# Performance work log

Measured on AMD Instinct MI355X. Metric: run time of the kernel, lower is better.

## Reference

```python
import jax, jax.numpy as jnp
import numpy as np

C, H, V, N, T = 1024, 256, 10000, 16, 256


def setup_inputs() -> dict:
    key = jax.random.key(0)
    ks = jax.random.split(key, 16)
    s = 1.0 / np.sqrt(H)
    rn = lambda k, shape, sc: (jax.random.normal(k, shape, dtype=jnp.float32) * sc)
    d = {}
    d["text"] = jax.random.randint(ks[0], (N, T), 0, V)
    d["start_emb"] = rn(ks[1], (C, H), 1.0)
    d["sw1"] = rn(ks[2], (H, H), s); d["sb1"] = jnp.zeros((H,), jnp.float32)
    d["sw2"] = rn(ks[3], (H, H), s); d["sb2"] = jnp.zeros((H,), jnp.float32)
    d["sw3"] = rn(ks[4], (H, 1), s); d["sb3"] = jnp.zeros((1,), jnp.float32)
    d["state_emb"] = rn(ks[5], (C, H), 1.0)
    d["tw1"] = rn(ks[6], (H, H), s); d["tb1"] = jnp.zeros((H,), jnp.float32)
    d["tw2"] = rn(ks[7], (H, H), s); d["tb2"] = jnp.zeros((H,), jnp.float32)
    d["tw3"] = rn(ks[8], (H, C), s); d["tb3"] = jnp.zeros((C,), jnp.float32)
    d["pre_emb"] = rn(ks[9], (C, H), 1.0)
    d["ew1"] = rn(ks[10], (H, H), s); d["eb1"] = jnp.zeros((H,), jnp.float32)
    d["ew2"] = rn(ks[11], (H, H), s); d["eb2"] = jnp.zeros((H,), jnp.float32)
    d["ew3"] = rn(ks[12], (H, V), s); d["eb3"] = jnp.zeros((V,), jnp.float32)
    return d


def _res(x, w1, b1, w2, b2):
    # ResidualLayerOld: relu(lin2(relu(lin1(x)))) + x
    return jax.nn.relu(jax.nn.relu(x @ w1 + b1) @ w2 + b2) + x


def reference(text, start_emb, sw1, sb1, sw2, sb2, sw3, sb3,
              state_emb, tw1, tb1, tw2, tb2, tw3, tb3,
              pre_emb, ew1, eb1, ew2, eb2, ew3, eb3):
    # start: [C] log p(z_0)
    start = jax.nn.log_softmax((_res(start_emb, sw1, sb1, sw2, sb2) @ sw3 + sb3)[:, 0])
    # transition: log_softmax over next state, then permute -> [next, prev]
    trans = jax.nn.log_softmax(_res(state_emb, tw1, tb1, tw2, tb2) @ tw3 + tb3, axis=-1).T
    # emission: log_softmax over vocab, permute -> [V, C]
    emit = jax.nn.log_softmax(_res(pre_emb, ew1, eb1, ew2, eb2) @ ew3 + eb3, axis=-1).T

    obs = emit[text]                      # [N, T, C] log p(x_t | z_t=c)
    alpha0 = start[None, :] + obs[:, 0]   # [N, C]

    def step(alpha, e_t):
        # log-semiring matvec: alpha'[n,j] = logsumexp_i alpha[n,i] + trans[j,i]
        a = jax.scipy.special.logsumexp(alpha[:, None, :] + trans[None, :, :], axis=-1) + e_t
        return a, None

    alpha, _ = jax.lax.scan(step, alpha0, jnp.swapaxes(obs, 0, 1)[1:])
    # evidence: logsumexp over final states, summed over batch (full lengths)
    return jax.scipy.special.logsumexp(alpha, axis=-1).sum()
```

## Files before the change

### kernel.cpp

```cpp
#include <hip/hip_runtime.h>
#include <hip/hip_bf16.h>
#include <cstddef>

#define CC 1024
#define HH 256
#define VV 10000
#define NN 16
#define TT 256
#define NB 16
#define NVB 40

typedef __attribute__((ext_vector_type(8))) short s8b;
typedef __attribute__((ext_vector_type(4))) float f32x4;
typedef __attribute__((ext_vector_type(4))) unsigned int u32x4;

__device__ __forceinline__ unsigned short f2bf(float f) {
    unsigned int b = __builtin_bit_cast(unsigned int, f);
    b += 0x7FFFu + ((b >> 16) & 1u);
    return (unsigned short)(b >> 16);
}
__device__ __forceinline__ float bf2f(unsigned short u) {
    return __builtin_bit_cast(float, ((unsigned int)u) << 16);
}

__global__ __launch_bounds__(256) void k_prep(
    const float* __restrict__ start_emb,
    const float* __restrict__ sw1, const float* __restrict__ sb1,
    const float* __restrict__ sw2, const float* __restrict__ sb2,
    const float* __restrict__ sw3, const float* __restrict__ sb3,
    const float* __restrict__ state_emb,
    const float* __restrict__ tw1, const float* __restrict__ tb1,
    const float* __restrict__ tw2, const float* __restrict__ tb2,
    const float* __restrict__ tw3, const float* __restrict__ tb3,
    const float* __restrict__ pre_emb,
    const float* __restrict__ ew1, const float* __restrict__ eb1,
    const float* __restrict__ ew2, const float* __restrict__ eb2,
    float* __restrict__ res_e, float* __restrict__ slog,
    unsigned short* __restrict__ PB, unsigned short* __restrict__ vbuf)
{
    __shared__ float xs[256][24];
    __shared__ float hs[256][24];
    const int th = threadIdx.x;
    const int b = blockIdx.x;

    if (b < 64) {
        const int r0 = b * 16;
        #pragma unroll
        for (int k = 0; k < 16; k++) xs[th][k] = pre_emb[(size_t)(r0 + k) * HH + th];
        __syncthreads();
        float acc[16];
        float b1v = eb1[th];
        #pragma unroll
        for (int r = 0; r < 16; r++) acc[r] = b1v;
        for (int h = 0; h < HH; h++) {
            float w = ew1[(size_t)h * HH + th];
            #pragma unroll
            for (int r = 0; r < 16; r++) acc[r] = fmaf(xs[h][r], w, acc[r]);
        }
        #pragma unroll
        for (int r = 0; r < 16; r++) hs[th][r] = fmaxf(acc[r], 0.f);
        __syncthreads();
        float b2v = eb2[th];
        #pragma unroll
        for (int r = 0; r < 16; r++) acc[r] = b2v;
        for (int h = 0; h < HH; h++) {
            float w = ew2[(size_t)h * HH + th];
            #pragma unroll
            for (int r = 0; r < 16; r++) acc[r] = fmaf(hs[h][r], w, acc[r]);
        }
        #pragma unroll
        for (int r = 0; r < 16; r++) {
            size_t idx = (size_t)(r0 + r) * HH + th;
            res_e[idx] = fmaxf(acc[r], 0.f) + pre_emb[idx];
        }
    } else if (b < 128) {
        const int r0 = (b - 64) * 16;
        #pragma unroll
        for (int k = 0; k < 16; k++) xs[th][k] = start_emb[(size_t)(r0 + k) * HH + th];
        __syncthreads();
        float acc[16];
        float b1v = sb1[th];
        #pragma unroll
        for (int r = 0; r < 16; r++) acc[r] = b1v;
        for (int h = 0; h < HH; h++) {
            float w = sw1[(size_t)h * HH + th];
            #pragma unroll
            for (int r = 0; r < 16; r++) acc[r] = fmaf(xs[h][r], w, acc[r]);
        }
        #pragma unroll
        for (int r = 0; r < 16; r++) hs[th][r] = fmaxf(acc[r], 0.f);
        __syncthreads();
        float b2v = sb2[th];
        #pragma unroll
        for (int r = 0; r < 16; r++) acc[r] = b2v;
        for (int h = 0; h < HH; h++) {
            float w = sw2[(size_t)h * HH + th];
            #pragma unroll
            for (int r = 0; r < 16; r++) acc[r] = fmaf(hs[h][r], w, acc[r]);
        }
        float accf[16];
        #pragma unroll
        for (int r = 0; r < 16; r++)
            accf[r] = fmaxf(acc[r], 0.f) + start_emb[(size_t)(r0 + r) * HH + th];
        __syncthreads();
        float* ws = (float*)&hs[0][0];
        float wv = sw3[th];
        const int wq = th >> 6, ln = th & 63;
        #pragma unroll
        for (int r = 0; r < 16; r++) {
            float p = accf[r] * wv;
            #pragma unroll
            for (int o = 32; o; o >>= 1) p += __shfl_xor(p, o);
            if (ln == 0) ws[wq * 16 + r] = p;
        }
        __syncthreads();
        if (th < 16) slog[r0 + th] = ws[th] + ws[16 + th] + ws[32 + th] + ws[48 + th] + sb3[0];
    } else if (b < 384) {
        const int r0c = (b - 128) * 4;
        float (*rs)[256] = (float (*)[256])&xs[0][0];
        float (*h2)[256] = (float (*)[256])(&xs[0][0] + 1024);
        float* sred = (float*)&hs[0][0];
        for (int k = 0; k < 4; k++) rs[k][th] = state_emb[(size_t)(r0c + k) * HH + th];
        __syncthreads();
        float a1[4];
        {
            float b1v = tb1[th];
            #pragma unroll
            for (int r = 0; r < 4; r++) a1[r] = b1v;
            for (int h = 0; h < HH; h++) {
                float w = tw1[(size_t)h * HH + th];
                #pragma unroll
                for (int r = 0; r < 4; r++) a1[r] = fmaf(rs[r][h], w, a1[r]);
            }
        }
        #pragma unroll
        for (int r = 0; r < 4; r++) h2[r][th] = fmaxf(a1[r], 0.f);
        __syncthreads();
        float a2[4];
        {
            float b2v = tb2[th];
            #pragma unroll
            for (int r = 0; r < 4; r++) a2[r] = b2v;
            for (int h = 0; h < HH; h++) {
                float w = tw2[(size_t)h * HH + th];
                #pragma unroll
                for (int r = 0; r < 4; r++) a2[r] = fmaf(h2[r][h], w, a2[r]);
            }
        }
        #pragma unroll
        for (int r = 0; r < 4; r++) rs[r][th] = fmaxf(a2[r], 0.f) + rs[r][th];
        __syncthreads();
        float acc[4][4];
        #pragma unroll
        for (int r = 0; r < 4; r++)
            #pragma unroll
            for (int q = 0; q < 4; q++) acc[r][q] = tb3[th + q * 256];
        for (int h = 0; h < HH; h++) {
            float w0 = tw3[(size_t)h * CC + th];
            float w1 = tw3[(size_t)h * CC + th + 256];
            float w2 = tw3[(size_t)h * CC + th + 512];
            float w3 = tw3[(size_t)h * CC + th + 768];
            #pragma unroll
            for (int r = 0; r < 4; r++) {
                float xv = rs[r][h];
                acc[r][0] = fmaf(xv, w0, acc[r][0]);
                acc[r][1] = fmaf(xv, w1, acc[r][1]);
                acc[r][2] = fmaf(xv, w2, acc[r][2]);
                acc[r][3] = fmaf(xv, w3, acc[r][3]);
            }
        }
        for (int r = 0; r < 4; r++) {
            float m = fmaxf(fmaxf(acc[r][0], acc[r][1]), fmaxf(acc[r][2], acc[r][3]));
            sred[th] = m; __syncthreads();
            for (int off = 128; off > 0; off >>= 1) { if (th < off) sred[th] = fmaxf(sred[th], sred[th + off]); __syncthreads(); }
            float rm = sred[0]; __syncthreads();
            float ssum = __expf(acc[r][0] - rm) + __expf(acc[r][1] - rm) + __expf(acc[r][2] - rm) + __expf(acc[r][3] - rm);
            sred[th] = ssum; __syncthreads();
            for (int off = 128; off > 0; off >>= 1) { if (th < off) sred[th] += sred[th + off]; __syncthreads(); }
            float inv = 1.0f / sred[0]; __syncthreads();
            #pragma unroll
            for (int q = 0; q < 4; q++) {
                float p = __expf(acc[r][q] - rm) * inv;
                PB[(size_t)(th + q * 256) * CC + (r0c + r)] = f2bf(p);
            }
        }
    } else {
        const int blk = b - 384;
        unsigned long long* dst = (unsigned long long*)vbuf + (size_t)blk * 16384;
        for (int i = th; i < 16384; i += 256) dst[i] = 0xFFFFFFFFFFFFFFFFull;
    }
}

__global__ __launch_bounds__(256) void k_emitg(const float* __restrict__ res_e,
                                               const float* __restrict__ ew3,
                                               const float* __restrict__ eb3,
                                               unsigned short* __restrict__ emitT,
                                               float* __restrict__ epart2)
{
    const int vb = blockIdx.x, c0 = blockIdx.y * 64;
    const int th = threadIdx.x;
    const int w = th >> 6, l = th & 63;
    const int lhi = l >> 4, llo = l & 15;
    const int wv = w & 1, wc = w >> 1;

    __shared__ __align__(16) unsigned short ewT[64 * 256];
    __shared__ __align__(16) unsigned short rsb[64 * 256];
    __shared__ float ebl[64];
    __shared__ float wlse[4][2][16][2];

    {
        char* base = (char*)rsb;
        #pragma unroll
        for (int i = 0; i < 8; i++) {
            int g = i * 2048 + th * 8;
            int row = g >> 8, h0 = g & 255;
            const float* src = res_e + (size_t)(c0 + row) * HH + h0;
            float4 f0 = *(const float4*)(src);
            float4 f1 = *(const float4*)(src + 4);
            s8b pk;
            pk[0] = (short)f2bf(f0.x); pk[1] = (short)f2bf(f0.y);
            pk[2] = (short)f2bf(f0.z); pk[3] = (short)f2bf(f0.w);
            pk[4] = (short)f2bf(f1.x); pk[5] = (short)f2bf(f1.y);
            pk[6] = (short)f2bf(f1.z); pk[7] = (short)f2bf(f1.w);
            *(s8b*)(base + row * 512 + ((h0 * 2) ^ ((row & 7) << 4))) = pk;
        }
    }

    float rM = -1e30f, rS = 0.f;

    for (int r = 0; r < 4; r++) {
        const int v0r = vb * 256 + r * 64;
        __syncthreads();
        {
            int tv = th & 63;
            char* base = (char*)ewT;
            int rowoff = tv * 512;
            int key = (tv & 7) << 4;
            int vglob = v0r + tv;
            bool valid = vglob < VV;
            #pragma unroll 8
            for (int i = 0; i < 64; i++) {
                int h = (th >> 6) + i * 4;
                float x = valid ? ew3[(size_t)h * VV + vglob] : 0.f;
                *(unsigned short*)(base + rowoff + ((h * 2) ^ key)) = f2bf(x);
            }
        }
        if (th < 64) ebl[th] = (v0r + th < VV) ? eb3[v0r + th] : 0.f;
        __syncthreads();

        f32x4 acc[2][2] = {{{0,0,0,0},{0,0,0,0}},{{0,0,0,0},{0,0,0,0}}};
        const char* ea = (const char*)ewT;
        const char* rb = (const char*)rsb;
        const int arow0 = wv * 32 + llo, arow1 = wv * 32 + 16 + llo;
        const int brow0 = wc * 32 + llo, brow1 = wc * 32 + 16 + llo;
        const int akey0 = (arow0 & 7) << 4;
        const int bkey0 = (brow0 & 7) << 4;
        #pragma unroll
        for (int kt = 0; kt < 8; kt++) {
            int off = kt * 64 + lhi * 16;
            s8b a0 = *(const s8b*)(ea + arow0 * 512 + (off ^ akey0));
            s8b a1 = *(const s8b*)(ea + arow1 * 512 + (off ^ akey0));
            s8b b0 = *(const s8b*)(rb + brow0 * 512 + (off ^ bkey0));
            s8b b1 = *(const s8b*)(rb + brow1 * 512 + (off ^ bkey0));
            acc[0][0] = __builtin_amdgcn_mfma_f32_16x16x32_bf16(a0, b0, acc[0][0], 0, 0, 0);
            acc[0][1] = __builtin_amdgcn_mfma_f32_16x16x32_bf16(a0, b1, acc[0][1], 0, 0, 0);
            acc[1][0] = __builtin_amdgcn_mfma_f32_16x16x32_bf16(a1, b0, acc[1][0], 0, 0, 0);
            acc[1][1] = __builtin_amdgcn_mfma_f32_16x16x32_bf16(a1, b1, acc[1][1], 0, 0, 0);
        }

        float um[2], us[2];
        #pragma unroll
        for (int u = 0; u < 2; u++) {
            float vals[8];
            #pragma unroll
            for (int s = 0; s < 2; s++) {
                #pragma unroll
                for (int q = 0; q < 4; q++) {
                    int vloc = wv * 32 + s * 16 + lhi * 4 + q;
                    int vglob = v0r + vloc;
                    float logit = acc[s][u][q] + ebl[vloc];
                    bool valid = vglob < VV;
                    if (valid)
                        emitT[(size_t)vglob * CC + (c0 + wc * 32 + u * 16 + llo)] = f2bf(logit);
                    vals[s * 4 + q] = valid ? logit : -1e30f;
                }
            }
            float m = vals[0];
            #pragma unroll
            for (int e = 1; e < 8; e++) m = fmaxf(m, vals[e]);
            float ss = 0.f;
            #pragma unroll
            for (int e = 0; e < 8; e++) ss += __expf(vals[e] - m);
            #pragma unroll
            for (int o = 16; o < 64; o <<= 1) {
                float m2 = __shfl_xor(m, o);
                float s2 = __shfl_xor(ss, o);
                float nm = fmaxf(m, m2);
                ss = ss * __expf(m - nm) + s2 * __expf(m2 - nm);
                m = nm;
            }
            um[u] = m; us[u] = ss;
        }
        if (l < 16) {
            #pragma unroll
            for (int u = 0; u < 2; u++) {
                wlse[w][u][l][0] = um[u];
                wlse[w][u][l][1] = us[u];
            }
        }
        __syncthreads();
        if (th < 64) {
            int wc2 = th >> 5, u2 = (th >> 4) & 1, ll2 = th & 15;
            float m1 = wlse[2 * wc2][u2][ll2][0], s1 = wlse[2 * wc2][u2][ll2][1];
            float m2 = wlse[2 * wc2 + 1][u2][ll2][0], s2 = wlse[2 * wc2 + 1][u2][ll2][1];
            float nm = fmaxf(m1, m2);
            float ns = s1 * __expf(m1 - nm) + s2 * __expf(m2 - nm);
            float fm = fmaxf(rM, nm);
            rS = rS * __expf(rM - fm) + ns * __expf(nm - fm);
            rM = fm;
        }
    }
    if (th < 64) {
        epart2[((size_t)vb * CC + c0 + th) * 2]     = rM;
        epart2[((size_t)vb * CC + c0 + th) * 2 + 1] = rS;
    }
}

__device__ __forceinline__ void load_stage(const unsigned short* vbuf_t, int th, char* vl)
{
    const unsigned short* sb = vbuf_t + th * 8;
    s8b ch[8];
    #pragma unroll
    for (int c = 0; c < 8; c++)
        asm volatile("global_load_dwordx4 %0, %1, off sc0 sc1"
                     : "=v"(ch[c]) : "v"(sb + c * 2048));
    asm volatile("s_waitcnt vmcnt(0)" ::: "memory");
    __builtin_amdgcn_sched_barrier(0);
    for (;;) {
        unsigned int miss = 0u;
        #pragma unroll
        for (int c = 0; c < 8; c++) {
            u32x4 d = __builtin_bit_cast(u32x4, ch[c]);
            if (d[0] == 0xFFFFFFFFu || d[1] == 0xFFFFFFFFu ||
                d[2] == 0xFFFFFFFFu || d[3] == 0xFFFFFFFFu) miss |= 1u << c;
        }
        if (!__any(miss != 0u)) break;
        #pragma unroll
        for (int c = 0; c < 8; c++)
            if (miss & (1u << c))
                asm volatile("global_load_dwordx4 %0, %1, off sc0 sc1"
                             : "=v"(ch[c]) : "v"(sb + c * 2048));
        asm volatile("s_waitcnt vmcnt(0)" ::: "memory");
        __builtin_amdgcn_sched_barrier(0);
    }
    #pragma unroll
    for (int c = 0; c < 8; c++) {
        int ow = c * 4096 + th * 16;
        *(s8b*)(vl + (ow ^ (((ow >> 11) & 7) << 4))) = ch[c];
    }
}

__global__ void __launch_bounds__(256, 1) k_fwd(
    const unsigned short* __restrict__ PB,
    const unsigned short* __restrict__ emitT,
    const float* __restrict__ epart2,
    const float* __restrict__ slog,
    const int* __restrict__ text,
    unsigned short* vbuf,
    float* __restrict__ outp)
{
    const int blk = blockIdx.x;
    const int th = threadIdx.x;
    const int w = th >> 6, l = th & 63;
    const int lhi = l >> 4, llo = l & 15;
    const int jglob = blk * 64 + w * 16 + llo;

    __shared__ int toks[NN * TT];
    __shared__ __align__(16) unsigned short vlds[NN * CC];
    __shared__ __align__(16) unsigned short vtile[16][72];
    __shared__ float swk[4];
    __shared__ float fin[16];
    __shared__ float lsej[64];

    for (int i = th; i < NN * TT; i += 256) toks[i] = text[i];

    s8b bfr[32];
    {
        const unsigned short* pbj = PB + (size_t)jglob * CC + lhi * 8;
        #pragma unroll
        for (int kt = 0; kt < 32; kt++)
            bfr[kt] = *(const s8b*)(pbj + kt * 32);
    }
    s8b ones;
    #pragma unroll
    for (int e = 0; e < 8; e++) ones[e] = (short)0x3F80;

    {
        float* mm  = (float*)vlds;
        float* ssm = mm + 256;
        int cl = blk * 64 + (th & 63);
        int v0 = (th >> 6) * 10;
        float M = -1e30f, S = 0.f;
        for (int vb = v0; vb < v0 + 10; vb++) {
            float m  = epart2[((size_t)vb * CC + cl) * 2];
            float s2 = epart2[((size_t)vb * CC + cl) * 2 + 1];
            float nm = fmaxf(M, m);
            S = S * __expf(M - nm) + s2 * __expf(m - nm);
            M = nm;
        }
        mm[th] = M; ssm[th] = S;
        __syncthreads();
        if (th < 64) {
            float Mf = -1e30f, Sf = 0.f;
            #pragma unroll
            for (int q = 0; q < 4; q++) {
                float m = mm[q * 64 + th], s2 = ssm[q * 64 + th];
                float nm = fmaxf(Mf, m);
                Sf = Sf * __expf(Mf - nm) + s2 * __expf(m - nm);
                Mf = nm;
            }
            lsej[th] = Mf + __logf(Sf);
        }
        __syncthreads();
    }
    const float lse_j = lsej[w * 16 + llo];

    float x0 = slog[th], x1 = slog[th + 256], x2 = slog[th + 512], x3 = slog[th + 768];
    float mw = fmaxf(fmaxf(x0, x1), fmaxf(x2, x3));
    #pragma unroll
    for (int o = 32; o; o >>= 1) mw = fmaxf(mw, __shfl_xor(mw, o));
    __syncthreads();
    if (l == 0) swk[w] = mw;
    __syncthreads();
    float gm = fmaxf(fmaxf(swk[0], swk[1]), fmaxf(swk[2], swk[3]));
    __syncthreads();
    float e4 = __expf(x0 - gm) + __expf(x1 - gm) + __expf(x2 - gm) + __expf(x3 - gm);
    #pragma unroll
    for (int o = 32; o; o >>= 1) e4 += __shfl_xor(e4, o);
    if (l == 0) swk[w] = e4;
    __syncthreads();
    float slse = gm + __logf(swk[0] + swk[1] + swk[2] + swk[3]);
    __syncthreads();

    if (th < 64) {
        int jj = blk * 64 + th;
        float p0 = __expf(slog[jj] - slse);
        float lsej_c = lsej[th];
        #pragma unroll
        for (int n = 0; n < 16; n++)
            vtile[n][th] = f2bf(p0 * __expf(bf2f(emitT[(size_t)toks[n * TT] * CC + jj]) - lsej_c));
    }
    __syncthreads();
    if (th < 128) {
        int n = th >> 3, seg = th & 7;
        s8b val = *(const s8b*)&vtile[n][seg * 8];
        unsigned short* dst = vbuf + (size_t)n * CC + blk * 64 + seg * 8;
        asm volatile("global_store_dwordx4 %0, %1, off sc0 sc1" :: "v"(dst), "v"(val) : "memory");
    }

    float logaccq[4] = {0.f, 0.f, 0.f, 0.f};
    char* vl = (char*)vlds;
    const int rkey = (llo & 7) << 4;
    const int rbase = llo * 2048 + lhi * 16;

    for (int t = 1; t < TT; t++) {
        float epf[4];
        #pragma unroll
        for (int q = 0; q < 4; q++)
            epf[q] = __expf(bf2f(emitT[(size_t)toks[(lhi * 4 + q) * TT + t] * CC + jglob]) - lse_j);

        load_stage(vbuf + (size_t)(t - 1) * (NN * CC), th, vl);
        __syncthreads();

        f32x4 ac0 = {0,0,0,0}, ac1 = {0,0,0,0}, ac2 = {0,0,0,0}, ac3 = {0,0,0,0};
        f32x4 ao0 = {0,0,0,0}, ao1 = {0,0,0,0};
        #pragma unroll
        for (int kt = 0; kt < 32; kt += 4) {
            s8b a0 = *(const s8b*)(vl + ((rbase + (kt + 0) * 64) ^ rkey));
            s8b a1 = *(const s8b*)(vl + ((rbase + (kt + 1) * 64) ^ rkey));
            s8b a2 = *(const s8b*)(vl + ((rbase + (kt + 2) * 64) ^ rkey));
            s8b a3 = *(const s8b*)(vl + ((rbase + (kt + 3) * 64) ^ rkey));
            ac0 = __builtin_amdgcn_mfma_f32_16x16x32_bf16(a0, bfr[kt + 0], ac0, 0, 0, 0);
            ao0 = __builtin_amdgcn_mfma_f32_16x16x32_bf16(a0, ones,        ao0, 0, 0, 0);
            ac1 = __builtin_amdgcn_mfma_f32_16x16x32_bf16(a1, bfr[kt + 1], ac1, 0, 0, 0);
            ao1 = __builtin_amdgcn_mfma_f32_16x16x32_bf16(a1, ones,        ao1, 0, 0, 0);
            ac2 = __builtin_amdgcn_mfma_f32_16x16x32_bf16(a2, bfr[kt + 2], ac2, 0, 0, 0);
            ao0 = __builtin_amdgcn_mfma_f32_16x16x32_bf16(a2, ones,        ao0, 0, 0, 0);
            ac3 = __builtin_amdgcn_mfma_f32_16x16x32_bf16(a3, bfr[kt + 3], ac3, 0, 0, 0);
            ao1 = __builtin_amdgcn_mfma_f32_16x16x32_bf16(a3, ones,        ao1, 0, 0, 0);
        }
        f32x4 acc = (ac0 + ac1) + (ac2 + ac3);
        f32x4 aco = ao0 + ao1;

        #pragma unroll
        for (int q = 0; q < 4; q++) {
            float S = aco[q];
            logaccq[q] += __logf(S);
            float vq = acc[q] * (1.0f / S) * epf[q];
            vtile[lhi * 4 + q][w * 16 + llo] = f2bf(vq);
        }
        __syncthreads();

        if (th < 128) {
            int n = th >> 3, seg = th & 7;
            s8b val = *(const s8b*)&vtile[n][seg * 8];
            unsigned short* dst = vbuf + (size_t)t * (NN * CC) + (size_t)n * CC + blk * 64 + seg * 8;
            asm volatile("global_store_dwordx4 %0, %1, off sc0 sc1" :: "v"(dst), "v"(val) : "memory");
        }
    }

    if (blk == 0) {
        load_stage(vbuf + (size_t)255 * (NN * CC), th, vl);
        __syncthreads();
        f32x4 ao0 = {0,0,0,0}, ao1 = {0,0,0,0};
        #pragma unroll
        for (int kt = 0; kt < 32; kt += 2) {
            s8b a0 = *(const s8b*)(vl + ((rbase + (kt + 0) * 64) ^ rkey));
            s8b a1 = *(const s8b*)(vl + ((rbase + (kt + 1) * 64) ^ rkey));
            ao0 = __builtin_amdgcn_mfma_f32_16x16x32_bf16(a0, ones, ao0, 0, 0, 0);
            ao1 = __builtin_amdgcn_mfma_f32_16x16x32_bf16(a1, ones, ao1, 0, 0, 0);
        }
        f32x4 acoF = ao0 + ao1;
        if (w == 0 && llo == 0) {
            #pragma unroll
            for (int q = 0; q < 4; q++)
                fin[lhi * 4 + q] = logaccq[q] + __logf(acoF[q]);
        }
        __syncthreads();
        if (th == 0) {
            float tot = 0.f;
            for (int n = 0; n < 16; n++) tot += fin[n];
            outp[0] = tot;
        }
    }
}

extern "C" void kernel_launch(void* const* d_in, const int* in_sizes, int n_in,
                              void* d_out, int out_size, void* d_ws, size_t ws_size,
                              hipStream_t stream) {
    const int*   text      = (const int*)  d_in[0];
    const float* start_emb = (const float*)d_in[1];
    const float* sw1 = (const float*)d_in[2];
    const float* sb1 = (const float*)d_in[3];
    const float* sw2 = (const float*)d_in[4];
    const float* sb2 = (const float*)d_in[5];
    const float* sw3 = (const float*)d_in[6];
    const float* sb3 = (const float*)d_in[7];
    const float* state_emb = (const float*)d_in[8];
    const float* tw1 = (const float*)d_in[9];
    const float* tb1 = (const float*)d_in[10];
    const float* tw2 = (const float*)d_in[11];
    const float* tb2 = (const float*)d_in[12];
    const float* tw3 = (const float*)d_in[13];
    const float* tb3 = (const float*)d_in[14];
    const float* pre_emb = (const float*)d_in[15];
    const float* ew1 = (const float*)d_in[16];
    const float* eb1 = (const float*)d_in[17];
    const float* ew2 = (const float*)d_in[18];
    const float* eb2 = (const float*)d_in[19];
    const float* ew3 = (const float*)d_in[20];
    const float* eb3 = (const float*)d_in[21];

    char* wsp = (char*)d_ws;
    unsigned short* PB    = (unsigned short*)(wsp);
    unsigned short* emitT = (unsigned short*)(wsp + ((size_t)2 << 20));
    float* res_e = (float*)(wsp + 22577152u);
    float* slog  = (float*)(wsp + 23625728u);
    float* epart2= (float*)(wsp + 23633920u);
    unsigned short* vbuf = (unsigned short*)(wsp + ((size_t)23 << 20));
    float* outp  = (float*)d_out;

    if (ws_size < ((size_t)31 << 20)) return;

    hipLaunchKernelGGL(k_prep,  dim3(448),     dim3(256), 0, stream,
                       start_emb, sw1, sb1, sw2, sb2, sw3, sb3,
                       state_emb, tw1, tb1, tw2, tb2, tw3, tb3,
                       pre_emb,   ew1, eb1, ew2, eb2,
                       res_e, slog, PB, vbuf);
    hipLaunchKernelGGL(k_emitg, dim3(NVB, 16), dim3(256), 0, stream, res_e, ew3, eb3, emitT, epart2);
    hipLaunchKernelGGL(k_fwd,   dim3(NB),      dim3(256), 0, stream,
                       PB, emitT, epart2, slog, text, vbuf, outp);
}
```

Before: 914.7 us.

## Halve forward-pass blocks to 8 with 512 threads and overlap emission loads

The persistent forward-recursion kernel now runs on 8 blocks of 512 threads, each covering 128 target states, instead of 16 blocks of 256. Fewer blocks take part in the per-step cross-block handoff through the global buffer, which is meant to cut polling and synchronisation cost on each of the 255 sequential steps. The emission gathers for a step are now issued alongside the stage loads, so their latency is hidden behind the same wait. In exchange each block does twice the MFMA work per step and runs 8 waves, which may raise per-step compute time and register pressure.

```diff
diff --git a/kernel.cpp b/kernel.cpp
--- a/kernel.cpp
+++ b/kernel.cpp
@@ -7,7 +7,7 @@
 #define VV 10000
 #define NN 16
 #define TT 256
-#define NB 16
+#define NB 8
 #define NVB 40
 
 typedef __attribute__((ext_vector_type(8))) short s8b;
@@ -326,41 +326,41 @@
     }
 }
 
-__device__ __forceinline__ void load_stage(const unsigned short* vbuf_t, int th, char* vl)
+__device__ __forceinline__ void load_stage512(const unsigned short* vbuf_t, int th, char* vl)
 {
     const unsigned short* sb = vbuf_t + th * 8;
-    s8b ch[8];
+    s8b ch[4];
     #pragma unroll
-    for (int c = 0; c < 8; c++)
+    for (int c = 0; c < 4; c++)
         asm volatile("global_load_dwordx4 %0, %1, off sc0 sc1"
-                     : "=v"(ch[c]) : "v"(sb + c * 2048));
+                     : "=v"(ch[c]) : "v"(sb + c * 4096));
     asm volatile("s_waitcnt vmcnt(0)" ::: "memory");
     __builtin_amdgcn_sched_barrier(0);
     for (;;) {
         unsigned int miss = 0u;
         #pragma unroll
-        for (int c = 0; c < 8; c++) {
+        for (int c = 0; c < 4; c++) {
             u32x4 d = __builtin_bit_cast(u32x4, ch[c]);
             if (d[0] == 0xFFFFFFFFu || d[1] == 0xFFFFFFFFu ||
                 d[2] == 0xFFFFFFFFu || d[3] == 0xFFFFFFFFu) miss |= 1u << c;
         }
         if (!__any(miss != 0u)) break;
         #pragma unroll
-        for (int c = 0; c < 8; c++)
+        for (int c = 0; c < 4; c++)
             if (miss & (1u << c))
                 asm volatile("global_load_dwordx4 %0, %1, off sc0 sc1"
-                             : "=v"(ch[c]) : "v"(sb + c * 2048));
+                             : "=v"(ch[c]) : "v"(sb + c * 4096));
         asm volatile("s_waitcnt vmcnt(0)" ::: "memory");
         __builtin_amdgcn_sched_barrier(0);
     }
     #pragma unroll
-    for (int c = 0; c < 8; c++) {
-        int ow = c * 4096 + th * 16;
+    for (int c = 0; c < 4; c++) {
+        int ow = c * 8192 + th * 16;
         *(s8b*)(vl + (ow ^ (((ow >> 11) & 7) << 4))) = ch[c];
     }
 }
 
-__global__ void __launch_bounds__(256, 1) k_fwd(
+__global__ void __launch_bounds__(512, 1) k_fwd(
     const unsigned short* __restrict__ PB,
     const unsigned short* __restrict__ emitT,
     const float* __restrict__ epart2,
@@ -373,16 +373,16 @@
     const int th = threadIdx.x;
     const int w = th >> 6, l = th & 63;
     const int lhi = l >> 4, llo = l & 15;
-    const int jglob = blk * 64 + w * 16 + llo;
+    const int jglob = blk * 128 + w * 16 + llo;
 
     __shared__ int toks[NN * TT];
     __shared__ __align__(16) unsigned short vlds[NN * CC];
-    __shared__ __align__(16) unsigned short vtile[16][72];
-    __shared__ float swk[4];
+    __shared__ __align__(16) unsigned short vtile[16][136];
+    __shared__ float swk[8];
     __shared__ float fin[16];
-    __shared__ float lsej[64];
-
-    for (int i = th; i < NN * TT; i += 256) toks[i] = text[i];
+    __shared__ float lsej[128];
+
+    for (int i = th; i < NN * TT; i += 512) toks[i] = text[i];
 
     s8b bfr[32];
     {
@@ -397,9 +397,9 @@
 
     {
         float* mm  = (float*)vlds;
-        float* ssm = mm + 256;
-        int cl = blk * 64 + (th & 63);
-        int v0 = (th >> 6) * 10;
+        float* ssm = mm + 512;
+        int cl = blk * 128 + (th & 127);
+        int v0 = (th >> 7) * 10;
         float M = -1e30f, S = 0.f;
         for (int vb = v0; vb < v0 + 10; vb++) {
             float m  = epart2[((size_t)vb * CC + cl) * 2];
@@ -410,11 +410,11 @@
         }
         mm[th] = M; ssm[th] = S;
         __syncthreads();
-        if (th < 64) {
+        if (th < 128) {
             float Mf = -1e30f, Sf = 0.f;
             #pragma unroll
             for (int q = 0; q < 4; q++) {
-                float m = mm[q * 64 + th], s2 = ssm[q * 64 + th];
+                float m = mm[q * 128 + th], s2 = ssm[q * 128 + th];
                 float nm = fmaxf(Mf, m);
                 Sf = Sf * __expf(Mf - nm) + s2 * __expf(m - nm);
                 Mf = nm;
@@ -425,25 +425,30 @@
     }
     const float lse_j = lsej[w * 16 + llo];
 
-    float x0 = slog[th], x1 = slog[th + 256], x2 = slog[th + 512], x3 = slog[th + 768];
-    float mw = fmaxf(fmaxf(x0, x1), fmaxf(x2, x3));
+    float x0 = slog[th], x1 = slog[th + 512];
+    float mw = fmaxf(x0, x1);
     #pragma unroll
     for (int o = 32; o; o >>= 1) mw = fmaxf(mw, __shfl_xor(mw, o));
     __syncthreads();
     if (l == 0) swk[w] = mw;
     __syncthreads();
-    float gm = fmaxf(fmaxf(swk[0], swk[1]), fmaxf(swk[2], swk[3]));
+    float gm = swk[0];
+    #pragma unroll
+    for (int q = 1; q < 8; q++) gm = fmaxf(gm, swk[q]);
     __syncthreads();
-    float e4 = __expf(x0 - gm) + __expf(x1 - gm) + __expf(x2 - gm) + __expf(x3 - gm);
+    float e2 = __expf(x0 - gm) + __expf(x1 - gm);
     #pragma unroll
-    for (int o = 32; o; o >>= 1) e4 += __shfl_xor(e4, o);
-    if (l == 0) swk[w] = e4;
+    for (int o = 32; o; o >>= 1) e2 += __shfl_xor(e2, o);
+    if (l == 0) swk[w] = e2;
     __syncthreads();
-    float slse = gm + __logf(swk[0] + swk[1] + swk[2] + swk[3]);
+    float ssum = swk[0];
+    #pragma unroll
+    for (int q = 1; q < 8; q++) ssum += swk[q];
+    float slse = gm + __logf(ssum);
     __syncthreads();
 
-    if (th < 64) {
-        int jj = blk * 64 + th;
+    if (th < 128) {
+        int jj = blk * 128 + th;
         float p0 = __expf(slog[jj] - slse);
         float lsej_c = lsej[th];
         #pragma unroll
@@ -451,10 +456,10 @@
             vtile[n][th] = f2bf(p0 * __expf(bf2f(emitT[(size_t)toks[n * TT] * CC + jj]) - lsej_c));
     }
     __syncthreads();
-    if (th < 128) {
-        int n = th >> 3, seg = th & 7;
+    if (th < 256) {
+        int n = th >> 4, seg = th & 15;
         s8b val = *(const s8b*)&vtile[n][seg * 8];
-        unsigned short* dst = vbuf + (size_t)n * CC + blk * 64 + seg * 8;
+        unsigned short* dst = vbuf + (size_t)n * CC + blk * 128 + seg * 8;
         asm volatile("global_store_dwordx4 %0, %1, off sc0 sc1" :: "v"(dst), "v"(val) : "memory");
     }
 
@@ -464,12 +469,45 @@
     const int rbase = llo * 2048 + lhi * 16;
 
     for (int t = 1; t < TT; t++) {
-        float epf[4];
-        #pragma unroll
-        for (int q = 0; q < 4; q++)
-            epf[q] = __expf(bf2f(emitT[(size_t)toks[(lhi * 4 + q) * TT + t] * CC + jglob]) - lse_j);
-
-        load_stage(vbuf + (size_t)(t - 1) * (NN * CC), th, vl);
+        const unsigned short* sb = vbuf + (size_t)(t - 1) * (NN * CC) + th * 8;
+        s8b ch[4];
+        #pragma unroll
+        for (int c = 0; c < 4; c++)
+            asm volatile("global_load_dwordx4 %0, %1, off sc0 sc1"
+                         : "=v"(ch[c]) : "v"(sb + c * 4096));
+
+        unsigned int epfu[4];
+        #pragma unroll
+        for (int q = 0; q < 4; q++) {
+            const unsigned short* ep = emitT + (size_t)toks[(lhi * 4 + q) * TT + t] * CC + jglob;
+            asm volatile("global_load_ushort %0, %1, off" : "=v"(epfu[q]) : "v"(ep));
+        }
+
+        asm volatile("s_waitcnt vmcnt(0)" ::: "memory");
+        __builtin_amdgcn_sched_barrier(0);
+        for (;;) {
+            unsigned int miss = 0u;
+            #pragma unroll
+            for (int c = 0; c < 4; c++) {
+                u32x4 d = __builtin_bit_cast(u32x4, ch[c]);
+                if (d[0] == 0xFFFFFFFFu || d[1] == 0xFFFFFFFFu ||
+                    d[2] == 0xFFFFFFFFu || d[3] == 0xFFFFFFFFu) miss |= 1u << c;
+            }
+            if (!__any(miss != 0u)) break;
+            #pragma unroll
+            for (int c = 0; c < 4; c++)
+                if (miss & (1u << c))
+                    asm volatile("global_load_dwordx4 %0, %1, off sc0 sc1"
+                                 : "=v"(ch[c]) : "v"(sb + c * 4096));
+            asm volatile("s_waitcnt vmcnt(0)" ::: "memory");
+            __builtin_amdgcn_sched_barrier(0);
+        }
+
+        #pragma unroll
+        for (int c = 0; c < 4; c++) {
+            int ow = c * 8192 + th * 16;
+            *(s8b*)(vl + (ow ^ (((ow >> 11) & 7) << 4))) = ch[c];
+        }
         __syncthreads();
 
         f32x4 ac0 = {0,0,0,0}, ac1 = {0,0,0,0}, ac2 = {0,0,0,0}, ac3 = {0,0,0,0};
@@ -496,21 +534,22 @@
         for (int q = 0; q < 4; q++) {
             float S = aco[q];
             logaccq[q] += __logf(S);
-            float vq = acc[q] * (1.0f / S) * epf[q];
+            float ep = __expf(bf2f((unsigned short)epfu[q]) - lse_j);
+            float vq = acc[q] * (1.0f / S) * ep;
             vtile[lhi * 4 + q][w * 16 + llo] = f2bf(vq);
         }
         __syncthreads();
 
-        if (th < 128) {
-            int n = th >> 3, seg = th & 7;
+        if (th < 256) {
+            int n = th >> 4, seg = th & 15;
             s8b val = *(const s8b*)&vtile[n][seg * 8];
-            unsigned short* dst = vbuf + (size_t)t * (NN * CC) + (size_t)n * CC + blk * 64 + seg * 8;
+            unsigned short* dst = vbuf + (size_t)t * (NN * CC) + (size_t)n * CC + blk * 128 + seg * 8;
             asm volatile("global_store_dwordx4 %0, %1, off sc0 sc1" :: "v"(dst), "v"(val) : "memory");
         }
     }
 
     if (blk == 0) {
-        load_stage(vbuf + (size_t)255 * (NN * CC), th, vl);
+        load_stage512(vbuf + (size_t)255 * (NN * CC), th, vl);
         __syncthreads();
         f32x4 ao0 = {0,0,0,0}, ao1 = {0,0,0,0};
         #pragma unroll
@@ -578,6 +617,6 @@
                        pre_emb,   ew1, eb1, ew2, eb2,
                        res_e, slog, PB, vbuf);
     hipLaunchKernelGGL(k_emitg, dim3(NVB, 16), dim3(256), 0, stream, res_e, ew3, eb3, emitT, epart2);
-    hipLaunchKernelGGL(k_fwd,   dim3(NB),      dim3(256), 0, stream,
+    hipLaunchKernelGGL(k_fwd,   dim3(NB),      dim3(512), 0, stream,
                        PB, emitT, epart2, slog, text, vbuf, outp);
 }
```

Result: slower. 951.9 us (+4.1%).

## Speculatively prefetch next step's alpha vector and poll for sentinel instead of barrier

Applied to the files above, without the earlier changes.

The forward recursion loop now issues the global loads for step t's alpha slice and emission values at the end of step t-1, overlapping them with the MFMA work. Correctness relies on a sentinel (0xFFFFFFFF) check: lanes that read unfinished data re-load until it is valid, which replaces the prior load_stage/grid-level wait. The scheme removes load latency from the critical path, but it depends on vbuf being pre-filled with the sentinel and on coherent sc0/sc1 loads, and it can spin.

```diff
diff --git a/kernel.cpp b/kernel.cpp
--- a/kernel.cpp
+++ b/kernel.cpp
@@ -463,14 +463,68 @@
     const int rkey = (llo & 7) << 4;
     const int rbase = llo * 2048 + lhi * 16;
 
+    s8b ch[8];
+    unsigned int epfu[4];
+    {
+        const unsigned short* sb0 = vbuf + th * 8;
+        #pragma unroll
+        for (int c = 0; c < 8; c++)
+            asm volatile("global_load_dwordx4 %0, %1, off sc0 sc1"
+                         : "=v"(ch[c]) : "v"(sb0 + c * 2048));
+        #pragma unroll
+        for (int q = 0; q < 4; q++) {
+            const unsigned short* ep = emitT + (size_t)toks[(lhi * 4 + q) * TT + 1] * CC + jglob;
+            asm volatile("global_load_ushort %0, %1, off" : "=v"(epfu[q]) : "v"(ep));
+        }
+    }
+
     for (int t = 1; t < TT; t++) {
-        float epf[4];
+        asm volatile("s_waitcnt vmcnt(0)" ::: "memory");
+        __builtin_amdgcn_sched_barrier(0);
+        {
+            const unsigned short* sb = vbuf + (size_t)(t - 1) * (NN * CC) + th * 8;
+            for (;;) {
+                unsigned int miss = 0u;
+                #pragma unroll
+                for (int c = 0; c < 8; c++) {
+                    u32x4 d = __builtin_bit_cast(u32x4, ch[c]);
+                    if (d[0] == 0xFFFFFFFFu || d[1] == 0xFFFFFFFFu ||
+                        d[2] == 0xFFFFFFFFu || d[3] == 0xFFFFFFFFu) miss |= 1u << c;
+                }
+                if (!__any(miss != 0u)) break;
+                #pragma unroll
+                for (int c = 0; c < 8; c++)
+                    if (miss & (1u << c))
+                        asm volatile("global_load_dwordx4 %0, %1, off sc0 sc1"
+                                     : "=v"(ch[c]) : "v"(sb + c * 2048));
+                asm volatile("s_waitcnt vmcnt(0)" ::: "memory");
+                __builtin_amdgcn_sched_barrier(0);
+            }
+        }
+        #pragma unroll
+        for (int c = 0; c < 8; c++) {
+            int ow = c * 4096 + th * 16;
+            *(s8b*)(vl + (ow ^ (((ow >> 11) & 7) << 4))) = ch[c];
+        }
+        __syncthreads();
+
+        float epv[4];
         #pragma unroll
         for (int q = 0; q < 4; q++)
-            epf[q] = __expf(bf2f(emitT[(size_t)toks[(lhi * 4 + q) * TT + t] * CC + jglob]) - lse_j);
-
-        load_stage(vbuf + (size_t)(t - 1) * (NN * CC), th, vl);
-        __syncthreads();
+            epv[q] = __expf(bf2f((unsigned short)epfu[q]) - lse_j);
+
+        if (t < TT - 1) {
+            #pragma unroll
+            for (int q = 0; q < 4; q++) {
+                const unsigned short* ep = emitT + (size_t)toks[(lhi * 4 + q) * TT + t + 1] * CC + jglob;
+                asm volatile("global_load_ushort %0, %1, off" : "=v"(epfu[q]) : "v"(ep));
+            }
+            const unsigned short* sbn = vbuf + (size_t)t * (NN * CC) + th * 8;
+            #pragma unroll
+            for (int c = 0; c < 8; c++)
+                asm volatile("global_load_dwordx4 %0, %1, off sc0 sc1"
+                             : "=v"(ch[c]) : "v"(sbn + c * 2048));
+        }
 
         f32x4 ac0 = {0,0,0,0}, ac1 = {0,0,0,0}, ac2 = {0,0,0,0}, ac3 = {0,0,0,0};
         f32x4 ao0 = {0,0,0,0}, ao1 = {0,0,0,0};
@@ -496,7 +550,7 @@
         for (int q = 0; q < 4; q++) {
             float S = aco[q];
             logaccq[q] += __logf(S);
-            float vq = acc[q] * (1.0f / S) * epf[q];
+            float vq = acc[q] * (1.0f / S) * epv[q];
             vtile[lhi * 4 + q][w * 16 + llo] = f2bf(vq);
         }
         __syncthreads();
```

Result: slower. 973.0 us (+6.4%).
